# Kernel optimization log

Hardware: AMD Instinct MI355X
Metric: run time of the kernel (lower is better)

The kernel has to match this reference:

```python
import jax, jax.numpy as jnp
import numpy as np
import jax.lax as lax

KERNEL = 7
STRIDE = 1
PAD = 3

def setup_inputs() -> dict:
    key = jax.random.key(0)
    kx, kw = jax.random.split(key)
    x = jax.random.normal(kx, (64, 512, 512), dtype=jnp.float32)
    weight = jax.random.normal(kw, (KERNEL, KERNEL), dtype=jnp.float32)
    return {"x": x, "weight": weight}

def reference(x, weight):
    # x: [B, H, W] single-channel; weight: [k, k]
    # Original computes cross-correlation (no kernel flip) with zero padding.
    lhs = x[:, None, :, :]                      # [B, 1, H, W]
    rhs = weight[None, None, :, :]              # [O=1, I=1, k, k]
    out = lax.conv_general_dilated(
        lhs, rhs,
        window_strides=(STRIDE, STRIDE),
        padding=[(PAD, PAD), (PAD, PAD)],
        dimension_numbers=("NCHW", "OIHW", "NCHW"),
    )
    return out[:, 0, :, :]                      # [B, H_out, W_out]
```

## Files before the change

kernel.cpp:

```cpp
#include <hip/hip_runtime.h>
#include <stdint.h>


#define IMG_W 512
#define IMG_H 512
#define NIMG  64
#define TW    256
#define TH    16
#define HALO  3
#define LDS_W 264
#define LDS_H (TH + 2*HALO)

__device__ __forceinline__ void gload_lds16(const float* src, float* dst_lds)
{
    __builtin_amdgcn_global_load_lds(
        (__attribute__((address_space(1))) void*)(uintptr_t)src,
        (__attribute__((address_space(3))) void*)(uintptr_t)dst_lds,
        16, 0, 0);
}

__global__ __launch_bounds__(256, 6) void conv7x7_kernel(
    const float* __restrict__ x,
    const float* __restrict__ wgt,
    float* __restrict__ out)
{
    __shared__ float tile[LDS_H * LDS_W];

    const int tid  = threadIdx.x;
    const int wave = tid >> 6;
    const int lane = tid & 63;
    const int bx   = blockIdx.x * TW;
    const int by   = blockIdx.y * TH;
    const int n    = blockIdx.z;

    const float* img = x + (size_t)n * (IMG_W * IMG_H);

    float w[49];
    #pragma unroll
    for (int i = 0; i < 49; ++i) w[i] = wgt[i];

    for (int r = wave; r < LDS_H; r += 4) {
        const int gy = by - HALO + r;
        float* dst = &tile[r * LDS_W + 4 + 4 * lane];
        if ((unsigned)gy < IMG_H) {
            gload_lds16(&img[(size_t)gy * IMG_W + bx + 4 * lane], dst);
        } else {
            *(float4*)dst = make_float4(0.f, 0.f, 0.f, 0.f);
        }
    }

    if (tid < 2 * LDS_H) {
        const int r    = tid >> 1;
        const int side = tid & 1;
        const int cb   = side ? (LDS_W - 4) : 0;
        const int gx   = side ? (bx + 256) : (bx - 4);
        const int gy   = by - HALO + r;
        float4 v = make_float4(0.f, 0.f, 0.f, 0.f);
        if (((unsigned)gy < IMG_H) && ((unsigned)gx < IMG_W))
            v = *(const float4*)&img[(size_t)gy * IMG_W + gx];
        *(float4*)&tile[r * LDS_W + cb] = v;
    }

    __syncthreads();

    const int lx = lane * 4;
    const int rbase = wave * 4;

    int d[6];
    #pragma unroll
    for (int t = 0; t < 6; ++t) {
        d[t] = t * 8;
        asm volatile("" : "+v"(d[t]));
    }

    const char* tb = (const char*)tile + (size_t)(rbase * LDS_W + lx) * 4;

    float acc[4][4] = {};
    float2 q[2][6];

    #pragma unroll
    for (int u = 0; u < 6; ++u)
        q[0][u] = *(const float2*)(tb + d[u]);

    #pragma unroll
    for (int r = 0; r < 10; ++r) {
        if (r < 9) {
            const char* rowb = tb + (size_t)(r + 1) * (LDS_W * 4);
            #pragma unroll
            for (int u = 0; u < 6; ++u)
                q[(r + 1) & 1][u] = *(const float2*)(rowb + d[u]);
        }

        const float2* qc = q[r & 1];
        const float row[12] = {qc[0].x, qc[0].y, qc[1].x, qc[1].y,
                               qc[2].x, qc[2].y, qc[3].x, qc[3].y,
                               qc[4].x, qc[4].y, qc[5].x, qc[5].y};
        #pragma unroll
        for (int j = 0; j < 4; ++j) {
            const int ky = r - j;
            if (ky >= 0 && ky < 7) {
                #pragma unroll
                for (int kx = 0; kx < 7; ++kx) {
                    const float wv = w[ky * 7 + kx];
                    #pragma unroll
                    for (int cc = 0; cc < 4; ++cc)
                        acc[j][cc] = fmaf(row[1 + kx + cc], wv, acc[j][cc]);
                }
            }
        }
    }

    float* o = out + (size_t)n * (IMG_W * IMG_H);
    #pragma unroll
    for (int j = 0; j < 4; ++j) {
        float4 v = make_float4(acc[j][0], acc[j][1], acc[j][2], acc[j][3]);
        *(float4*)&o[(size_t)(by + rbase + j) * IMG_W + bx + lx] = v;
    }
}

extern "C" void kernel_launch(void* const* d_in, const int* in_sizes, int n_in,
                              void* d_out, int out_size, void* d_ws, size_t ws_size,
                              hipStream_t stream)
{
    const float* x   = (const float*)d_in[0];
    const float* wgt = (const float*)d_in[1];
    float* out       = (float*)d_out;

    dim3 grid(IMG_W / TW, IMG_H / TH, NIMG);
    conv7x7_kernel<<<grid, 256, 0, stream>>>(x, wgt, out);
}
```

Measured before the change: 118.0 us.

## Give each wave a private LDS halo region and drop block barrier

Each wave now loads its own 10-row window (4 output rows plus a 3-row halo on each side) into a private LDS region. The wave waits only on its own memory counters instead of a block-wide __syncthreads. The grid is flattened to one dimension with a swizzled block-to-tile mapping, intended to spread neighbouring tiles across XCDs and improve L2 locality. The cost is more redundant halo loading, since 40 rows are loaded instead of 22, and a larger LDS footprint, so launch bounds drop to 3 blocks per CU.

```diff
diff --git a/kernel.cpp b/kernel.cpp
--- a/kernel.cpp
+++ b/kernel.cpp
@@ -8,8 +8,9 @@
 #define TW    256
 #define TH    16
 #define HALO  3
-#define LDS_W 264
-#define LDS_H (TH + 2*HALO)
+#define WROWS 10
+#define RW    264
+#define WREG  (WROWS * RW)
 
 __device__ __forceinline__ void gload_lds16(const float* src, float* dst_lds)
 {
@@ -19,52 +20,62 @@
         16, 0, 0);
 }
 
-__global__ __launch_bounds__(256, 6) void conv7x7_kernel(
+__global__ __launch_bounds__(256, 3) void conv7x7_kernel(
     const float* __restrict__ x,
     const float* __restrict__ wgt,
     float* __restrict__ out)
 {
-    __shared__ float tile[LDS_H * LDS_W];
+    __shared__ float lds[4 * WREG];
 
     const int tid  = threadIdx.x;
     const int wave = tid >> 6;
     const int lane = tid & 63;
-    const int bx   = blockIdx.x * TW;
-    const int by   = blockIdx.y * TH;
-    const int n    = blockIdx.z;
+
+    const int id = blockIdx.x;
+    const int l  = (id & 7) * 512 + (id >> 3);
+    const int ty = l & 31;
+    const int s  = l >> 5;
+    const int bx = (s & 1) * TW;
+    const int n  = s >> 1;
+    const int by = ty * TH;
 
     const float* img = x + (size_t)n * (IMG_W * IMG_H);
+    float* o = out + (size_t)n * (IMG_W * IMG_H);
 
     float w[49];
     #pragma unroll
     for (int i = 0; i < 49; ++i) w[i] = wgt[i];
 
-    for (int r = wave; r < LDS_H; r += 4) {
-        const int gy = by - HALO + r;
-        float* dst = &tile[r * LDS_W + 4 + 4 * lane];
-        if ((unsigned)gy < IMG_H) {
-            gload_lds16(&img[(size_t)gy * IMG_W + bx + 4 * lane], dst);
-        } else {
-            *(float4*)dst = make_float4(0.f, 0.f, 0.f, 0.f);
-        }
+    float* reg = &lds[wave * WREG];
+    const int gy0 = by + wave * 4 - HALO;
+
+    const bool edge = (lane < 2 * WROWS);
+    const int  er   = lane >> 1;
+    const int  es   = lane & 1;
+    float4 ev = make_float4(0.f, 0.f, 0.f, 0.f);
+    if (edge) {
+        const int gx = es ? (bx + TW) : (bx - 4);
+        const int gy = gy0 + er;
+        if (((unsigned)gy < IMG_H) && ((unsigned)gx < IMG_W))
+            ev = *(const float4*)&img[(size_t)gy * IMG_W + gx];
     }
 
-    if (tid < 2 * LDS_H) {
-        const int r    = tid >> 1;
-        const int side = tid & 1;
-        const int cb   = side ? (LDS_W - 4) : 0;
-        const int gx   = side ? (bx + 256) : (bx - 4);
-        const int gy   = by - HALO + r;
-        float4 v = make_float4(0.f, 0.f, 0.f, 0.f);
-        if (((unsigned)gy < IMG_H) && ((unsigned)gx < IMG_W))
-            v = *(const float4*)&img[(size_t)gy * IMG_W + gx];
-        *(float4*)&tile[r * LDS_W + cb] = v;
+    #pragma unroll
+    for (int r = 0; r < WROWS; ++r) {
+        const int gy = gy0 + r;
+        float* dst = reg + r * RW + 4 + 4 * lane;
+        if ((unsigned)gy < IMG_H)
+            gload_lds16(&img[(size_t)gy * IMG_W + bx + 4 * lane], dst);
+        else
+            *(float4*)dst = make_float4(0.f, 0.f, 0.f, 0.f);
     }
 
-    __syncthreads();
+    asm volatile("s_waitcnt vmcnt(0)" ::: "memory");
 
-    const int lx = lane * 4;
-    const int rbase = wave * 4;
+    if (edge)
+        *(float4*)(reg + er * RW + (es ? (RW - 4) : 0)) = ev;
+
+    asm volatile("s_waitcnt lgkmcnt(0)" ::: "memory");
 
     int d[6];
     #pragma unroll
@@ -73,7 +84,7 @@
         asm volatile("" : "+v"(d[t]));
     }
 
-    const char* tb = (const char*)tile + (size_t)(rbase * LDS_W + lx) * 4;
+    const char* tb = (const char*)reg + (size_t)lane * 16;
 
     float acc[4][4] = {};
     float2 q[2][6];
@@ -85,7 +96,7 @@
     #pragma unroll
     for (int r = 0; r < 10; ++r) {
         if (r < 9) {
-            const char* rowb = tb + (size_t)(r + 1) * (LDS_W * 4);
+            const char* rowb = tb + (size_t)(r + 1) * (RW * 4);
             #pragma unroll
             for (int u = 0; u < 6; ++u)
                 q[(r + 1) & 1][u] = *(const float2*)(rowb + d[u]);
@@ -110,11 +121,10 @@
         }
     }
 
-    float* o = out + (size_t)n * (IMG_W * IMG_H);
     #pragma unroll
     for (int j = 0; j < 4; ++j) {
         float4 v = make_float4(acc[j][0], acc[j][1], acc[j][2], acc[j][3]);
-        *(float4*)&o[(size_t)(by + rbase + j) * IMG_W + bx + lx] = v;
+        *(float4*)&o[(size_t)(by + wave * 4 + j) * IMG_W + bx + lane * 4] = v;
     }
 }
 
@@ -126,6 +136,6 @@
     const float* wgt = (const float*)d_in[1];
     float* out       = (float*)d_out;
 
-    dim3 grid(IMG_W / TW, IMG_H / TH, NIMG);
+    dim3 grid(4096);
     conv7x7_kernel<<<grid, 256, 0, stream>>>(x, wgt, out);
 }
```

New measurement: 124.7 us. +5.7%, slower.
